# Optimization experiments

Measured on AMD Instinct MI355X. Metric: run time of the kernel, lower is better.

The kernel has to match this reference:

```python
import jax, jax.numpy as jnp
import numpy as np

B, L, E, H, FF = 2, 2048, 1024, 16, 4096
DH = E // H
EPS = 1e-5
# NOTE: source has attn_scale = 1 / dh**(-0.5) == sqrt(dh) (multiplies, not divides)
ATTN_SCALE = float(DH) ** 0.5


def _layernorm(x, w, b):
    mu = jnp.mean(x, axis=-1, keepdims=True)
    var = jnp.mean((x - mu) ** 2, axis=-1, keepdims=True)
    return (x - mu) * jax.lax.rsqrt(var + EPS) * w + b


def setup_inputs() -> dict:
    key = jax.random.key(0)
    ks = jax.random.split(key, 8)
    s = 0.02
    return {
        "x": jax.random.normal(ks[0], (B, L, E), jnp.float32),
        "ln1_w": jnp.ones((E,), jnp.float32),
        "ln1_b": jnp.zeros((E,), jnp.float32),
        "wq": jax.random.normal(ks[1], (E, E), jnp.float32) * s,
        "bq": jnp.zeros((E,), jnp.float32),
        "wk": jax.random.normal(ks[2], (E, E), jnp.float32) * s,
        "bk": jnp.zeros((E,), jnp.float32),
        "wv": jax.random.normal(ks[3], (E, E), jnp.float32) * s,
        "bv": jnp.zeros((E,), jnp.float32),
        "wo": jax.random.normal(ks[4], (E, E), jnp.float32) * s,
        "bo": jnp.zeros((E,), jnp.float32),
        "ln2_w": jnp.ones((E,), jnp.float32),
        "ln2_b": jnp.zeros((E,), jnp.float32),
        "wu": jax.random.normal(ks[5], (E, FF), jnp.float32) * s,
        "bu": jnp.zeros((FF,), jnp.float32),
        "wd": jax.random.normal(ks[6], (FF, E), jnp.float32) * s,
        "bd": jnp.zeros((E,), jnp.float32),
    }


def reference(x, ln1_w, ln1_b, wq, bq, wk, bk, wv, bv, wo, bo,
              ln2_w, ln2_b, wu, bu, wd, bd):
    # --- attention block (pre-LN, manual softmax attention) ---
    xn = _layernorm(x, ln1_w, ln1_b)                       # [B,L,E]
    q = (xn @ wq + bq).reshape(B, L, H, DH)
    k = (xn @ wk + bk).reshape(B, L, H, DH)
    v = (xn @ wv + bv).reshape(B, L, H, DH)
    score = jnp.einsum("blhd,bmhd->bhlm", q, k) * ATTN_SCALE  # [B,H,L,L]
    attn = jax.nn.softmax(score, axis=-1)
    ctx = jnp.einsum("bhlm,bmhd->blhd", attn, v).reshape(B, L, E)
    hidden = x + (ctx @ wo + bo)
    # --- FFN block (pre-LN, GELU) ---
    hn = _layernorm(hidden, ln2_w, ln2_b)
    up = jax.nn.gelu(hn @ wu + bu, approximate=False)      # [B,L,F]
    down = up @ wd + bd
    return hidden + down
```

## Files before the change

### kernel.cpp

```cpp
#include <hip/hip_runtime.h>
#include <stdint.h>


typedef __attribute__((ext_vector_type(8))) short short8;
typedef __attribute__((ext_vector_type(4))) float floatx4;

extern "C" __device__ float __ocml_native_exp2_f32(float);
#define EXP2(x) __ocml_native_exp2_f32(x)

#define MFMA_BF16(a, b, c) __builtin_amdgcn_mfma_f32_16x16x32_bf16((a), (b), (c), 0, 0, 0)

__device__ __forceinline__ unsigned short f2bf(float f) {
  union { float f; unsigned int u; } v; v.f = f;
  unsigned int r = v.u + 0x7FFFu + ((v.u >> 16) & 1u);
  return (unsigned short)(r >> 16);
}

__device__ __forceinline__ unsigned int f2u(float f) {
  union { float f; unsigned int u; } v; v.f = f; return v.u;
}

__device__ __forceinline__ void gl_lds16(const unsigned short* g, unsigned short* l) {
  __builtin_amdgcn_global_load_lds(
      (const __attribute__((address_space(1))) unsigned int*)g,
      (__attribute__((address_space(3))) unsigned int*)l, 16, 0, 0);
}

template <int MODE, int BN>
__global__ __launch_bounds__(256)
void gemm_bt(const unsigned short* __restrict__ A,
             const unsigned short* __restrict__ Bt,
             const float* __restrict__ bias,
             void* __restrict__ outp,
             const float* __restrict__ res,
             int K,
             void* __restrict__ out2, void* __restrict__ out3,
             const float* __restrict__ bias2, const float* __restrict__ bias3) {
  constexpr int BM = 128, BK = 64;
  constexpr int MI = (BN == 128) ? 4 : 2;
  constexpr int NI = 4;
  __shared__ __align__(16) unsigned short As[BM * BK];
  __shared__ __align__(16) unsigned short Bs[BN * BK];
  const int tid = threadIdx.x;
  const int wave = tid >> 6, lane = tid & 63, l16 = lane & 15, quad = lane >> 4;
  const int m0 = blockIdx.y * BM, n0 = blockIdx.x * BN;
  const int wm = (BN == 128) ? (wave >> 1) * 64 : wave * 32;
  const int wn = (BN == 128) ? (wave & 1) * 64 : 0;
  const int sw = l16 & 7;
  const int sl0 = (quad ^ sw) << 3;
  const int sl1 = sl0 ^ 32;

  floatx4 acc[MI][NI] = {};

  for (int k0 = 0; k0 < K; k0 += BK) {
    __syncthreads();
#pragma unroll
    for (int c = 0; c < (BM * BK) / 2048; ++c) {
      const int e = (c * 256 + tid) * 8;
      const int row = e >> 6, c8 = (e >> 3) & 7;
      gl_lds16(A + (size_t)(m0 + row) * K + k0 + ((c8 ^ (row & 7)) << 3), &As[e]);
    }
#pragma unroll
    for (int c = 0; c < (BN * BK) / 2048; ++c) {
      const int e = (c * 256 + tid) * 8;
      const int row = e >> 6, c8 = (e >> 3) & 7;
      gl_lds16(Bt + (size_t)(n0 + row) * K + k0 + ((c8 ^ (row & 7)) << 3), &Bs[e]);
    }
    __syncthreads();

    short8 af0[MI], af1[MI], bf0[NI], bf1[NI];
#pragma unroll
    for (int i = 0; i < MI; ++i) {
      af0[i] = *(const short8*)&As[(wm + i * 16 + l16) * BK + sl0];
      af1[i] = *(const short8*)&As[(wm + i * 16 + l16) * BK + sl1];
    }
#pragma unroll
    for (int i = 0; i < NI; ++i) {
      bf0[i] = *(const short8*)&Bs[(wn + i * 16 + l16) * BK + sl0];
      bf1[i] = *(const short8*)&Bs[(wn + i * 16 + l16) * BK + sl1];
    }
#pragma unroll
    for (int mi = 0; mi < MI; ++mi)
#pragma unroll
      for (int ni = 0; ni < NI; ++ni) {
        acc[mi][ni] = MFMA_BF16(af0[mi], bf0[ni], acc[mi][ni]);
        acc[mi][ni] = MFMA_BF16(af1[mi], bf1[ni], acc[mi][ni]);
      }
  }

  const int seg = (MODE == 0) ? (n0 >> 10) : 0;
  const float* bptr = bias;
  if constexpr (MODE == 0) bptr = (seg == 0) ? bias : (seg == 1 ? bias2 : bias3);

  float bcol[NI];
#pragma unroll
  for (int ni = 0; ni < NI; ++ni) {
    const int n = n0 + wn + ni * 16 + l16;
    bcol[ni] = bptr[(MODE == 0) ? (n & 1023) : n];
  }

#pragma unroll
  for (int mi = 0; mi < MI; ++mi) {
#pragma unroll
    for (int r = 0; r < 4; ++r) {
      const int m = m0 + wm + mi * 16 + quad * 4 + r;
#pragma unroll
      for (int ni = 0; ni < NI; ++ni) {
        const int n = n0 + wn + ni * 16 + l16;
        const float c = acc[mi][ni][r] + bcol[ni];
        if constexpr (MODE == 0) {
          const int b_ = m >> 11, l = m & 2047, hd = n & 1023;
          const size_t idx =
              ((size_t)((b_ * 16 + (hd >> 6)) * 2048 + l)) * 64 + (hd & 63);
          if (seg == 0)       ((unsigned short*)outp)[idx] = f2bf(c * 11.5415603270f);
          else if (seg == 1)  ((unsigned short*)out2)[idx] = f2bf(c);
          else                ((unsigned short*)out3)[idx] = f2bf(c);
        } else if constexpr (MODE == 1) {
          ((float*)outp)[(size_t)m * 1024 + n] = res[(size_t)m * 1024 + n] + c;
        } else if constexpr (MODE == 2) {
          const float g = 0.5f * c * (1.0f + erff(c * 0.70710678118654752f));
          ((unsigned short*)outp)[(size_t)m * 4096 + n] = f2bf(g);
        } else {
          ((float*)outp)[(size_t)m * 1024 + n] = res[(size_t)m * 1024 + n] + c;
        }
      }
    }
  }
}

__global__ __launch_bounds__(256)
void layernorm_kernel(const float* __restrict__ x, const float* __restrict__ w,
                      const float* __restrict__ b, unsigned short* __restrict__ out) {
  const int row = blockIdx.x, tid = threadIdx.x;
  const int wave = tid >> 6, lane = tid & 63;
  const float4 v = ((const float4*)(x + (size_t)row * 1024))[tid];
  float s = v.x + v.y + v.z + v.w;
  float s2 = v.x * v.x + v.y * v.y + v.z * v.z + v.w * v.w;
#pragma unroll
  for (int off = 32; off > 0; off >>= 1) {
    s += __shfl_down(s, off);
    s2 += __shfl_down(s2, off);
  }
  __shared__ float red[8];
  if (lane == 0) { red[wave] = s; red[4 + wave] = s2; }
  __syncthreads();
  const float ts = red[0] + red[1] + red[2] + red[3];
  const float ts2 = red[4] + red[5] + red[6] + red[7];
  const float mu = ts * (1.0f / 1024.0f);
  const float var = ts2 * (1.0f / 1024.0f) - mu * mu;
  const float rs = rsqrtf(var + 1e-5f);
  const float4 wv = ((const float4*)w)[tid];
  const float4 bv = ((const float4*)b)[tid];
  ushort4 o;
  o.x = f2bf((v.x - mu) * rs * wv.x + bv.x);
  o.y = f2bf((v.y - mu) * rs * wv.y + bv.y);
  o.z = f2bf((v.z - mu) * rs * wv.z + bv.z);
  o.w = f2bf((v.w - mu) * rs * wv.w + bv.w);
  ((ushort4*)(out + (size_t)row * 1024))[tid] = o;
}

__global__ __launch_bounds__(256)
void transpose_cast4(const float* __restrict__ s0, const float* __restrict__ s1,
                     const float* __restrict__ s2, const float* __restrict__ s3,
                     unsigned short* __restrict__ dst) {
  __shared__ float tile[32][33];
  const int z = blockIdx.z;
  const float* in = (z == 0) ? s0 : (z == 1) ? s1 : (z == 2) ? s2 : s3;
  unsigned short* out = dst + (size_t)z * 1024 * 1024;
  const int tx = threadIdx.x, ty = threadIdx.y;
  const int c0 = blockIdx.x * 32, r0 = blockIdx.y * 32;
#pragma unroll
  for (int i = 0; i < 4; ++i)
    tile[ty + 8 * i][tx] = in[(size_t)(r0 + ty + 8 * i) * 1024 + c0 + tx];
  __syncthreads();
#pragma unroll
  for (int i = 0; i < 4; ++i)
    out[(size_t)(c0 + ty + 8 * i) * 1024 + r0 + tx] = f2bf(tile[tx][ty + 8 * i]);
}

__global__ __launch_bounds__(256)
void transpose_cast(const float* __restrict__ in, unsigned short* __restrict__ out,
                    int R, int C) {
  __shared__ float tile[32][33];
  const int tx = threadIdx.x, ty = threadIdx.y;
  const int c0 = blockIdx.x * 32, r0 = blockIdx.y * 32;
#pragma unroll
  for (int i = 0; i < 4; ++i)
    tile[ty + 8 * i][tx] = in[(size_t)(r0 + ty + 8 * i) * C + c0 + tx];
  __syncthreads();
#pragma unroll
  for (int i = 0; i < 4; ++i)
    out[(size_t)(c0 + ty + 8 * i) * R + r0 + tx] = f2bf(tile[tx][ty + 8 * i]);
}

__global__ __launch_bounds__(256)
void transpose_bf16(const unsigned short* __restrict__ in,
                    unsigned short* __restrict__ out, int R, int C) {
  __shared__ unsigned short tile[32][33];
  const size_t hoff = (size_t)blockIdx.z * R * C;
  in += hoff; out += hoff;
  const int tx = threadIdx.x, ty = threadIdx.y;
  const int c0 = blockIdx.x * 32, r0 = blockIdx.y * 32;
#pragma unroll
  for (int i = 0; i < 4; ++i)
    tile[ty + 8 * i][tx] = in[(size_t)(r0 + ty + 8 * i) * C + c0 + tx];
  __syncthreads();
#pragma unroll
  for (int i = 0; i < 4; ++i)
    out[(size_t)(c0 + ty + 8 * i) * R + r0 + tx] = tile[tx][ty + 8 * i];
}

__global__ __launch_bounds__(256)
void flash_attn(const unsigned short* __restrict__ q,
                const unsigned short* __restrict__ k,
                const unsigned short* __restrict__ v,
                unsigned short* __restrict__ ctx) {
  __shared__ __align__(16) unsigned short Ks[2][64 * 64];
  __shared__ __align__(16) unsigned short Vs[2][64 * 64];
  __shared__ __align__(16) unsigned short Ps[4][2][16 * 72];
  const int bh = blockIdx.y, qt = blockIdx.x;
  const int tid = threadIdx.x, wave = tid >> 6, lane = tid & 63;
  const int l16 = lane & 15, quad = lane >> 4;
  const unsigned short* kb = k + (size_t)bh * 2048 * 64;
  const unsigned short* vb = v + (size_t)bh * 64 * 2048;

  int qrow[2];
  short8 qf0[2], qf1[2];
#pragma unroll
  for (int g = 0; g < 2; ++g) {
    qrow[g] = qt * 128 + g * 64 + wave * 16 + l16;
    const unsigned short* qp = q + (size_t)bh * 2048 * 64 + (size_t)qrow[g] * 64;
    qf0[g] = *(const short8*)(qp + quad * 8);
    qf1[g] = *(const short8*)(qp + 32 + quad * 8);
  }

  floatx4 O[2][4] = {};
  float m_run[2] = {-1e30f, -1e30f}, l_run[2] = {0.f, 0.f};

  auto stage = [&](int t, int bufi) {
    const int kv0 = t * 64;
#pragma unroll
    for (int c = 0; c < 2; ++c) {
      const int e = (c * 256 + tid) * 8;
      const int r = e >> 6, ch = (e >> 3) & 7;
      const int sc = ((ch ^ (r & 7)) << 3);
      gl_lds16(kb + (size_t)(kv0 + r) * 64 + sc, &Ks[bufi][e]);
      gl_lds16(vb + (size_t)r * 2048 + kv0 + sc, &Vs[bufi][e]);
    }
  };
  stage(0, 0);

  const int sw = l16 & 7;
  const int sl0 = (quad ^ sw) << 3, sl1 = sl0 ^ 32;

  for (int t = 0; t < 32; ++t) {
    __syncthreads();
    const int bufi = t & 1;
    if (t + 1 < 32) stage(t + 1, bufi ^ 1);

    floatx4 st[2][4];
#pragma unroll
    for (int nt = 0; nt < 4; ++nt) {
      const int r0 = (nt * 16 + l16) * 64;
      const short8 kf0 = *(const short8*)&Ks[bufi][r0 + sl0];
      const short8 kf1 = *(const short8*)&Ks[bufi][r0 + sl1];
#pragma unroll
      for (int g = 0; g < 2; ++g) {
        floatx4 z = {};
        z = MFMA_BF16(kf0, qf0[g], z);
        z = MFMA_BF16(kf1, qf1[g], z);
        st[g][nt] = z;
      }
    }

    short8 pf0[2], pf1[2];
#pragma unroll
    for (int g = 0; g < 2; ++g) {
      float mx = st[g][0][0];
#pragma unroll
      for (int nt = 0; nt < 4; ++nt)
#pragma unroll
        for (int r = 0; r < 4; ++r) mx = fmaxf(mx, st[g][nt][r]);
      mx = fmaxf(mx, __shfl_xor(mx, 16));
      mx = fmaxf(mx, __shfl_xor(mx, 32));
      const float m_new = fmaxf(m_run[g], mx);
      const float alpha = EXP2(m_run[g] - m_new);
      m_run[g] = m_new;

      float rsum = 0.f;
#pragma unroll
      for (int nt = 0; nt < 4; ++nt) {
        const float p0 = EXP2(st[g][nt][0] - m_new);
        const float p1 = EXP2(st[g][nt][1] - m_new);
        const float p2 = EXP2(st[g][nt][2] - m_new);
        const float p3 = EXP2(st[g][nt][3] - m_new);
        rsum += (p0 + p1) + (p2 + p3);
        uint2 pk;
        pk.x = __builtin_amdgcn_perm(f2u(p1), f2u(p0), 0x07060302u);
        pk.y = __builtin_amdgcn_perm(f2u(p3), f2u(p2), 0x07060302u);
        *(uint2*)&Ps[wave][g][l16 * 72 + nt * 16 + quad * 4] = pk;
      }
      rsum += __shfl_xor(rsum, 16);
      rsum += __shfl_xor(rsum, 32);
      l_run[g] = l_run[g] * alpha + rsum;

#pragma unroll
      for (int nt = 0; nt < 4; ++nt) {
        O[g][nt][0] *= alpha; O[g][nt][1] *= alpha;
        O[g][nt][2] *= alpha; O[g][nt][3] *= alpha;
      }
      pf0[g] = *(const short8*)&Ps[wave][g][l16 * 72 + quad * 8];
      pf1[g] = *(const short8*)&Ps[wave][g][l16 * 72 + 32 + quad * 8];
    }

#pragma unroll
    for (int nt = 0; nt < 4; ++nt) {
      const int r0 = (nt * 16 + l16) * 64;
      const short8 vf0 = *(const short8*)&Vs[bufi][r0 + sl0];
      const short8 vf1 = *(const short8*)&Vs[bufi][r0 + sl1];
#pragma unroll
      for (int g = 0; g < 2; ++g) {
        O[g][nt] = MFMA_BF16(vf0, pf0[g], O[g][nt]);
        O[g][nt] = MFMA_BF16(vf1, pf1[g], O[g][nt]);
      }
    }
  }

  const int b_ = bh >> 4, h = bh & 15;
#pragma unroll
  for (int g = 0; g < 2; ++g) {
    const float inv = 1.0f / l_run[g];
    unsigned short* op = ctx + ((size_t)(b_ * 2048) + qrow[g]) * 1024 + h * 64;
#pragma unroll
    for (int nt = 0; nt < 4; ++nt) {
      ushort4 o4;
      o4.x = f2bf(O[g][nt][0] * inv);
      o4.y = f2bf(O[g][nt][1] * inv);
      o4.z = f2bf(O[g][nt][2] * inv);
      o4.w = f2bf(O[g][nt][3] * inv);
      *(ushort4*)(op + nt * 16 + quad * 4) = o4;
    }
  }
}

extern "C" void kernel_launch(void* const* d_in, const int* in_sizes, int n_in,
                              void* d_out, int out_size, void* d_ws, size_t ws_size,
                              hipStream_t stream) {
  const float* x     = (const float*)d_in[0];
  const float* ln1_w = (const float*)d_in[1];
  const float* ln1_b = (const float*)d_in[2];
  const float* wq    = (const float*)d_in[3];
  const float* bq    = (const float*)d_in[4];
  const float* wk    = (const float*)d_in[5];
  const float* bk    = (const float*)d_in[6];
  const float* wv    = (const float*)d_in[7];
  const float* bv    = (const float*)d_in[8];
  const float* wo    = (const float*)d_in[9];
  const float* bo    = (const float*)d_in[10];
  const float* ln2_w = (const float*)d_in[11];
  const float* ln2_b = (const float*)d_in[12];
  const float* wu    = (const float*)d_in[13];
  const float* bu    = (const float*)d_in[14];
  const float* wd    = (const float*)d_in[15];
  const float* bd    = (const float*)d_in[16];

  char* W = (char*)d_ws;
  const size_t MB = 1ull << 20;
  unsigned short* wqkvT = (unsigned short*)(W + 0 * MB);
  unsigned short* woT   = (unsigned short*)(W + 6 * MB);
  unsigned short* wuT   = (unsigned short*)(W + 8 * MB);
  unsigned short* wdT   = (unsigned short*)(W + 16 * MB);
  unsigned short* xn    = (unsigned short*)(W + 24 * MB);
  unsigned short* qb    = (unsigned short*)(W + 32 * MB);
  unsigned short* kb    = (unsigned short*)(W + 40 * MB);
  unsigned short* vb    = (unsigned short*)(W + 48 * MB);
  unsigned short* cx    = (unsigned short*)(W + 56 * MB);
  float*          hid   = (float*)(W + 64 * MB);
  unsigned short* up    = (unsigned short*)(W + 24 * MB);

  const dim3 tb(32, 8);
  transpose_cast4<<<dim3(32, 32, 4), tb, 0, stream>>>(wq, wk, wv, wo, wqkvT);
  transpose_cast<<<dim3(128, 32), tb, 0, stream>>>(wu, wuT, 1024, 4096);
  transpose_cast<<<dim3(32, 128), tb, 0, stream>>>(wd, wdT, 4096, 1024);

  layernorm_kernel<<<4096, 256, 0, stream>>>(x, ln1_w, ln1_b, xn);
  gemm_bt<0, 128><<<dim3(24, 32), 256, 0, stream>>>(
      xn, wqkvT, bq, qb, nullptr, 1024, kb, cx, bk, bv);
  transpose_bf16<<<dim3(2, 64, 32), tb, 0, stream>>>(cx, vb, 2048, 64);
  flash_attn<<<dim3(16, 32), 256, 0, stream>>>(qb, kb, vb, cx);
  gemm_bt<1, 64><<<dim3(16, 32), 256, 0, stream>>>(
      cx, woT, bo, hid, x, 1024, nullptr, nullptr, nullptr, nullptr);

  layernorm_kernel<<<4096, 256, 0, stream>>>(hid, ln2_w, ln2_b, cx);
  gemm_bt<2, 128><<<dim3(32, 32), 256, 0, stream>>>(
      cx, wuT, bu, up, nullptr, 1024, nullptr, nullptr, nullptr, nullptr);
  gemm_bt<3, 64><<<dim3(16, 32), 256, 0, stream>>>(
      up, wdT, bd, d_out, hid, 4096, nullptr, nullptr, nullptr, nullptr);
}
```

Measured before the change: 380.6 us.

## Double-buffer GEMM LDS tiles with halved K-step to overlap loads and MFMA

The GEMM main loop now keeps two LDS buffers with a K-tile of 32 instead of one buffer with 64, so total shared memory stays the same. It prefetches the next tile with global_load_lds while computing on the current one, removing one of the two barriers per iteration. The XOR swizzle is reworked to fit the 32-wide rows. In exchange it runs twice as many loop iterations and barriers. The overlap may be lost if the compiler inserts a vmcnt wait before the LDS reads.

```diff
diff --git a/kernel.cpp b/kernel.cpp
--- a/kernel.cpp
+++ b/kernel.cpp
@@ -36,56 +36,59 @@
              int K,
              void* __restrict__ out2, void* __restrict__ out3,
              const float* __restrict__ bias2, const float* __restrict__ bias3) {
-  constexpr int BM = 128, BK = 64;
+  constexpr int BM = 128, BK = 32;
   constexpr int MI = (BN == 128) ? 4 : 2;
   constexpr int NI = 4;
-  __shared__ __align__(16) unsigned short As[BM * BK];
-  __shared__ __align__(16) unsigned short Bs[BN * BK];
+  __shared__ __align__(16) unsigned short As[2][BM * BK];
+  __shared__ __align__(16) unsigned short Bs[2][BN * BK];
   const int tid = threadIdx.x;
   const int wave = tid >> 6, lane = tid & 63, l16 = lane & 15, quad = lane >> 4;
   const int m0 = blockIdx.y * BM, n0 = blockIdx.x * BN;
   const int wm = (BN == 128) ? (wave >> 1) * 64 : wave * 32;
   const int wn = (BN == 128) ? (wave & 1) * 64 : 0;
-  const int sw = l16 & 7;
-  const int sl0 = (quad ^ sw) << 3;
-  const int sl1 = sl0 ^ 32;
+  const int sA = (l16 >> 1) & 3;
+  const int slot = (quad ^ sA) << 3;
 
   floatx4 acc[MI][NI] = {};
 
-  for (int k0 = 0; k0 < K; k0 += BK) {
-    __syncthreads();
+  auto stage = [&](int t, int bufi) {
+    const int k0 = t * BK;
 #pragma unroll
     for (int c = 0; c < (BM * BK) / 2048; ++c) {
       const int e = (c * 256 + tid) * 8;
-      const int row = e >> 6, c8 = (e >> 3) & 7;
-      gl_lds16(A + (size_t)(m0 + row) * K + k0 + ((c8 ^ (row & 7)) << 3), &As[e]);
+      const int row = e >> 5, c4 = (e >> 3) & 3;
+      gl_lds16(A + (size_t)(m0 + row) * K + k0 + ((c4 ^ ((row >> 1) & 3)) << 3),
+               &As[bufi][e]);
     }
 #pragma unroll
     for (int c = 0; c < (BN * BK) / 2048; ++c) {
       const int e = (c * 256 + tid) * 8;
-      const int row = e >> 6, c8 = (e >> 3) & 7;
-      gl_lds16(Bt + (size_t)(n0 + row) * K + k0 + ((c8 ^ (row & 7)) << 3), &Bs[e]);
-    }
+      const int row = e >> 5, c4 = (e >> 3) & 3;
+      gl_lds16(Bt + (size_t)(n0 + row) * K + k0 + ((c4 ^ ((row >> 1) & 3)) << 3),
+               &Bs[bufi][e]);
+    }
+  };
+
+  const int nIter = K / BK;
+  stage(0, 0);
+
+  for (int t = 0; t < nIter; ++t) {
     __syncthreads();
-
-    short8 af0[MI], af1[MI], bf0[NI], bf1[NI];
-#pragma unroll
-    for (int i = 0; i < MI; ++i) {
-      af0[i] = *(const short8*)&As[(wm + i * 16 + l16) * BK + sl0];
-      af1[i] = *(const short8*)&As[(wm + i * 16 + l16) * BK + sl1];
-    }
-#pragma unroll
-    for (int i = 0; i < NI; ++i) {
-      bf0[i] = *(const short8*)&Bs[(wn + i * 16 + l16) * BK + sl0];
-      bf1[i] = *(const short8*)&Bs[(wn + i * 16 + l16) * BK + sl1];
-    }
+    const int bufi = t & 1;
+    if (t + 1 < nIter) stage(t + 1, bufi ^ 1);
+
+    short8 af[MI], bf[NI];
+#pragma unroll
+    for (int i = 0; i < MI; ++i)
+      af[i] = *(const short8*)&As[bufi][(wm + i * 16 + l16) * BK + slot];
+#pragma unroll
+    for (int i = 0; i < NI; ++i)
+      bf[i] = *(const short8*)&Bs[bufi][(wn + i * 16 + l16) * BK + slot];
 #pragma unroll
     for (int mi = 0; mi < MI; ++mi)
 #pragma unroll
-      for (int ni = 0; ni < NI; ++ni) {
-        acc[mi][ni] = MFMA_BF16(af0[mi], bf0[ni], acc[mi][ni]);
-        acc[mi][ni] = MFMA_BF16(af1[mi], bf1[ni], acc[mi][ni]);
-      }
+      for (int ni = 0; ni < NI; ++ni)
+        acc[mi][ni] = MFMA_BF16(af[mi], bf[ni], acc[mi][ni]);
   }
 
   const int seg = (MODE == 0) ? (n0 >> 10) : 0;
```

Measured after the change: 401.0 us. +5.3%, slower.

## Split-K the FFN down GEMM, use 64x64 tiles for Wo, shrink attention LDS

Applied to the files above, without the earlier changes.

The FFN down-projection now runs as a 2-way split-K GEMM that writes two fp32 partial buffers. A new elementwise kernel sums the partials with the bias and the residual. The output-projection GEMM switches to 64x64 tiles, doubling its block count, and flash attention reuses a single P staging buffer per wave to cut LDS use. The aim is more parallelism and occupancy on the large-K GEMM. The cost is extra global traffic for the fp32 partials plus one more kernel launch.

```diff
diff --git a/kernel.cpp b/kernel.cpp
--- a/kernel.cpp
+++ b/kernel.cpp
@@ -26,45 +26,52 @@
       (__attribute__((address_space(3))) unsigned int*)l, 16, 0, 0);
 }
 
-template <int MODE, int BN>
+template <int MODE, int BM, int BN>
 __global__ __launch_bounds__(256)
 void gemm_bt(const unsigned short* __restrict__ A,
              const unsigned short* __restrict__ Bt,
              const float* __restrict__ bias,
              void* __restrict__ outp,
              const float* __restrict__ res,
-             int K,
+             int Ksub, int lda,
              void* __restrict__ out2, void* __restrict__ out3,
              const float* __restrict__ bias2, const float* __restrict__ bias3) {
-  constexpr int BM = 128, BK = 64;
-  constexpr int MI = (BN == 128) ? 4 : 2;
-  constexpr int NI = 4;
+  constexpr int BK = 64;
+  constexpr int MI = (BM == 128 && BN == 128) ? 4 : 2;
+  constexpr int NI = (BM == 64) ? 2 : 4;
   __shared__ __align__(16) unsigned short As[BM * BK];
   __shared__ __align__(16) unsigned short Bs[BN * BK];
   const int tid = threadIdx.x;
   const int wave = tid >> 6, lane = tid & 63, l16 = lane & 15, quad = lane >> 4;
   const int m0 = blockIdx.y * BM, n0 = blockIdx.x * BN;
-  const int wm = (BN == 128) ? (wave >> 1) * 64 : wave * 32;
-  const int wn = (BN == 128) ? (wave & 1) * 64 : 0;
+  const int kbase = blockIdx.z * Ksub;
+
+  int wm, wn;
+  if constexpr (BM == 128 && BN == 128) { wm = (wave >> 1) * 64; wn = (wave & 1) * 64; }
+  else if constexpr (BM == 128)         { wm = wave * 32;        wn = 0; }
+  else                                  { wm = (wave >> 1) * 32; wn = (wave & 1) * 32; }
+
   const int sw = l16 & 7;
   const int sl0 = (quad ^ sw) << 3;
   const int sl1 = sl0 ^ 32;
 
   floatx4 acc[MI][NI] = {};
 
-  for (int k0 = 0; k0 < K; k0 += BK) {
+  for (int k0 = 0; k0 < Ksub; k0 += BK) {
     __syncthreads();
 #pragma unroll
     for (int c = 0; c < (BM * BK) / 2048; ++c) {
       const int e = (c * 256 + tid) * 8;
       const int row = e >> 6, c8 = (e >> 3) & 7;
-      gl_lds16(A + (size_t)(m0 + row) * K + k0 + ((c8 ^ (row & 7)) << 3), &As[e]);
+      gl_lds16(A + (size_t)(m0 + row) * lda + kbase + k0 + ((c8 ^ (row & 7)) << 3),
+               &As[e]);
     }
 #pragma unroll
     for (int c = 0; c < (BN * BK) / 2048; ++c) {
       const int e = (c * 256 + tid) * 8;
       const int row = e >> 6, c8 = (e >> 3) & 7;
-      gl_lds16(Bt + (size_t)(n0 + row) * K + k0 + ((c8 ^ (row & 7)) << 3), &Bs[e]);
+      gl_lds16(Bt + (size_t)(n0 + row) * lda + kbase + k0 + ((c8 ^ (row & 7)) << 3),
+               &Bs[e]);
     }
     __syncthreads();
 
@@ -95,9 +102,15 @@
   float bcol[NI];
 #pragma unroll
   for (int ni = 0; ni < NI; ++ni) {
-    const int n = n0 + wn + ni * 16 + l16;
-    bcol[ni] = bptr[(MODE == 0) ? (n & 1023) : n];
-  }
+    if constexpr (MODE == 4) { bcol[ni] = 0.f; }
+    else {
+      const int n = n0 + wn + ni * 16 + l16;
+      bcol[ni] = bptr[(MODE == 0) ? (n & 1023) : n];
+    }
+  }
+
+  float* const pdst = (MODE == 4)
+      ? ((blockIdx.z == 0) ? (float*)outp : (float*)out2) : (float*)outp;
 
 #pragma unroll
   for (int mi = 0; mi < MI; ++mi) {
@@ -121,11 +134,29 @@
           const float g = 0.5f * c * (1.0f + erff(c * 0.70710678118654752f));
           ((unsigned short*)outp)[(size_t)m * 4096 + n] = f2bf(g);
         } else {
-          ((float*)outp)[(size_t)m * 1024 + n] = res[(size_t)m * 1024 + n] + c;
+          pdst[(size_t)m * 1024 + n] = c;
         }
       }
     }
   }
+}
+
+__global__ __launch_bounds__(256)
+void ffn_down_combine(const float* __restrict__ hid, const float* __restrict__ bd,
+                      const float* __restrict__ p0, const float* __restrict__ p1,
+                      float* __restrict__ out) {
+  const int idx = blockIdx.x * 256 + threadIdx.x;
+  const int col4 = idx & 255;
+  const float4 h = ((const float4*)hid)[idx];
+  const float4 b = ((const float4*)bd)[col4];
+  const float4 a = ((const float4*)p0)[idx];
+  const float4 c = ((const float4*)p1)[idx];
+  float4 o;
+  o.x = h.x + b.x + a.x + c.x;
+  o.y = h.y + b.y + a.y + c.y;
+  o.z = h.z + b.z + a.z + c.z;
+  o.w = h.w + b.w + a.w + c.w;
+  ((float4*)out)[idx] = o;
 }
 
 __global__ __launch_bounds__(256)
@@ -217,7 +248,7 @@
                 unsigned short* __restrict__ ctx) {
   __shared__ __align__(16) unsigned short Ks[2][64 * 64];
   __shared__ __align__(16) unsigned short Vs[2][64 * 64];
-  __shared__ __align__(16) unsigned short Ps[4][2][16 * 72];
+  __shared__ __align__(16) unsigned short Ps[4][16 * 72];
   const int bh = blockIdx.y, qt = blockIdx.x;
   const int tid = threadIdx.x, wave = tid >> 6, lane = tid & 63;
   const int l16 = lane & 15, quad = lane >> 4;
@@ -298,7 +329,7 @@
         uint2 pk;
         pk.x = __builtin_amdgcn_perm(f2u(p1), f2u(p0), 0x07060302u);
         pk.y = __builtin_amdgcn_perm(f2u(p3), f2u(p2), 0x07060302u);
-        *(uint2*)&Ps[wave][g][l16 * 72 + nt * 16 + quad * 4] = pk;
+        *(uint2*)&Ps[wave][l16 * 72 + nt * 16 + quad * 4] = pk;
       }
       rsum += __shfl_xor(rsum, 16);
       rsum += __shfl_xor(rsum, 32);
@@ -309,8 +340,8 @@
         O[g][nt][0] *= alpha; O[g][nt][1] *= alpha;
         O[g][nt][2] *= alpha; O[g][nt][3] *= alpha;
       }
-      pf0[g] = *(const short8*)&Ps[wave][g][l16 * 72 + quad * 8];
-      pf1[g] = *(const short8*)&Ps[wave][g][l16 * 72 + 32 + quad * 8];
+      pf0[g] = *(const short8*)&Ps[wave][l16 * 72 + quad * 8];
+      pf1[g] = *(const short8*)&Ps[wave][l16 * 72 + 32 + quad * 8];
     }
 
 #pragma unroll
@@ -366,6 +397,7 @@
 
   char* W = (char*)d_ws;
   const size_t MB = 1ull << 20;
+  float*          p0    = (float*)(W + 0 * MB);
   unsigned short* wqkvT = (unsigned short*)(W + 0 * MB);
   unsigned short* woT   = (unsigned short*)(W + 6 * MB);
   unsigned short* wuT   = (unsigned short*)(W + 8 * MB);
@@ -377,6 +409,7 @@
   unsigned short* cx    = (unsigned short*)(W + 56 * MB);
   float*          hid   = (float*)(W + 64 * MB);
   unsigned short* up    = (unsigned short*)(W + 24 * MB);
+  float*          p1    = (float*)(W + 80 * MB);
 
   const dim3 tb(32, 8);
   transpose_cast4<<<dim3(32, 32, 4), tb, 0, stream>>>(wq, wk, wv, wo, wqkvT);
@@ -384,16 +417,17 @@
   transpose_cast<<<dim3(32, 128), tb, 0, stream>>>(wd, wdT, 4096, 1024);
 
   layernorm_kernel<<<4096, 256, 0, stream>>>(x, ln1_w, ln1_b, xn);
-  gemm_bt<0, 128><<<dim3(24, 32), 256, 0, stream>>>(
-      xn, wqkvT, bq, qb, nullptr, 1024, kb, cx, bk, bv);
+  gemm_bt<0, 128, 128><<<dim3(24, 32), 256, 0, stream>>>(
+      xn, wqkvT, bq, qb, nullptr, 1024, 1024, kb, cx, bk, bv);
   transpose_bf16<<<dim3(2, 64, 32), tb, 0, stream>>>(cx, vb, 2048, 64);
   flash_attn<<<dim3(16, 32), 256, 0, stream>>>(qb, kb, vb, cx);
-  gemm_bt<1, 64><<<dim3(16, 32), 256, 0, stream>>>(
-      cx, woT, bo, hid, x, 1024, nullptr, nullptr, nullptr, nullptr);
+  gemm_bt<1, 64, 64><<<dim3(16, 64), 256, 0, stream>>>(
+      cx, woT, bo, hid, x, 1024, 1024, nullptr, nullptr, nullptr, nullptr);
 
   layernorm_kernel<<<4096, 256, 0, stream>>>(hid, ln2_w, ln2_b, cx);
-  gemm_bt<2, 128><<<dim3(32, 32), 256, 0, stream>>>(
-      cx, wuT, bu, up, nullptr, 1024, nullptr, nullptr, nullptr, nullptr);
-  gemm_bt<3, 64><<<dim3(16, 32), 256, 0, stream>>>(
-      up, wdT, bd, d_out, hid, 4096, nullptr, nullptr, nullptr, nullptr);
-}
+  gemm_bt<2, 128, 128><<<dim3(32, 32), 256, 0, stream>>>(
+      cx, wuT, bu, up, nullptr, 1024, 1024, nullptr, nullptr, nullptr, nullptr);
+  gemm_bt<4, 128, 64><<<dim3(16, 32, 2), 256, 0, stream>>>(
+      up, wdT, nullptr, p0, nullptr, 2048, 4096, p1, nullptr, nullptr, nullptr);
+  ffn_down_combine<<<4096, 256, 0, stream>>>(hid, bd, p0, p1, (float*)d_out);
+}
```

Result: no change. 388.0 us (+1.9%).
